# Kernel optimization log

Hardware: AMD Instinct MI355X
Metric: run time of the kernel (lower is better)

The kernel has to match this reference:

```python
import jax, jax.numpy as jnp
import numpy as np

DEPTH = 5
EPS = 1e-8


def setup_inputs() -> dict:
    key = jax.random.key(0)
    ks = jax.random.split(key, 7)
    N, E, Q = 50000, 1600000, 16
    return {
        "marg_i": jax.random.normal(ks[0], (N, Q), dtype=jnp.float32),
        "cav_ij": jax.random.uniform(ks[1], (E, Q), dtype=jnp.float32),
        "C": jax.random.uniform(ks[2], (Q, Q), dtype=jnp.float32),
        "field_i": jax.random.normal(ks[3], (N, Q), dtype=jnp.float32),
        "edge_dst": jax.random.randint(ks[4], (E,), 0, N, dtype=jnp.int32),
        "a1_src": jax.random.randint(ks[5], (E,), 0, N, dtype=jnp.int32),
        "indice_ij": jax.random.randint(ks[6], (E,), 0, E, dtype=jnp.int32),
    }


def reference(marg_i, cav_ij, C, field_i, edge_dst, a1_src, indice_ij):
    # Belief-propagation layers repeated DEPTH times.
    # B_ @ temp2  -> segment_sum of edge messages into destination nodes [N,Q]
    # A1 @ marg_i -> gather of source-node marginal per edge [E,Q]
    N = field_i.shape[0]

    def step(carry, _):
        marg, cav = carry
        temp2 = jnp.log(cav @ C + EPS)                                  # [E,Q]
        marg = jax.ops.segment_sum(temp2, edge_dst, num_segments=N) + field_i  # [N,Q]
        cav = jax.nn.softmax(marg[a1_src] - temp2[indice_ij], axis=1)  # [E,Q]
        return (marg, cav), None

    (marg, cav), _ = jax.lax.scan(step, (marg_i, cav_ij), None, length=DEPTH)
    return jax.nn.log_softmax(marg, axis=1)
```

## Files before the change

### kernel.cpp

```cpp
#include <hip/hip_runtime.h>
#include <hip/hip_fp16.h>

#define Q 16
#define EPS 1e-8f
#define DEPTH 5

typedef unsigned int u32;
typedef _Float16 h2 __attribute__((ext_vector_type(2)));

__device__ __forceinline__ u32 pack2(float a, float b) {
    __half2 h = __floats2half2_rn(a, b);
    return *(u32*)&h;
}
__device__ __forceinline__ float2 unpack2(u32 u) {
    __half2 h = *(__half2*)&u;
    return __half22float2(h);
}
__device__ __forceinline__ h2 mkh2(float a, float b) {
    h2 v; v[0] = (_Float16)a; v[1] = (_Float16)b; return v;
}


__global__ __launch_bounds__(256) void hist_kernel(
    const int* __restrict__ dst, int* __restrict__ count, int E)
{
    int e = blockIdx.x * 256 + threadIdx.x;
    if (e < E) atomicAdd(&count[dst[e]], 1);
}

__global__ __launch_bounds__(256) void scan_partial(
    const int* __restrict__ count, int* __restrict__ partial, int N)
{
    __shared__ int sm[256];
    int i = blockIdx.x * 256 + threadIdx.x;
    sm[threadIdx.x] = (i < N) ? count[i] : 0;
    __syncthreads();
    for (int off = 128; off > 0; off >>= 1) {
        if (threadIdx.x < off) sm[threadIdx.x] += sm[threadIdx.x + off];
        __syncthreads();
    }
    if (threadIdx.x == 0) partial[blockIdx.x] = sm[0];
}

__global__ __launch_bounds__(1024) void scan_top(
    int* __restrict__ partial, int nb)
{
    __shared__ int sm[1024];
    int t = threadIdx.x;
    int v = (t < nb) ? partial[t] : 0;
    sm[t] = v;
    __syncthreads();
    for (int off = 1; off < 1024; off <<= 1) {
        int u = (t >= off) ? sm[t - off] : 0;
        __syncthreads();
        sm[t] += u;
        __syncthreads();
    }
    if (t < nb) partial[t] = sm[t] - v;
}

__global__ __launch_bounds__(256) void scan_final(
    const int* __restrict__ count, const int* __restrict__ partial,
    int* __restrict__ start, int N)
{
    __shared__ int sm[256];
    int i = blockIdx.x * 256 + threadIdx.x;
    int v = (i < N) ? count[i] : 0;
    sm[threadIdx.x] = v;
    __syncthreads();
    for (int off = 1; off < 256; off <<= 1) {
        int u = (threadIdx.x >= off) ? sm[threadIdx.x - off] : 0;
        __syncthreads();
        sm[threadIdx.x] += u;
        __syncthreads();
    }
    int excl = sm[threadIdx.x] - v + partial[blockIdx.x];
    if (i < N) start[i] = excl;
    if (i == N - 1) start[N] = excl + v;
}

__global__ __launch_bounds__(256) void rank_kernel(
    const int* __restrict__ dst, int* __restrict__ cursor,
    int* __restrict__ pos, int E)
{
    int e = blockIdx.x * 256 + threadIdx.x;
    if (e < E) pos[e] = atomicAdd(&cursor[dst[e]], 1);
}

__global__ __launch_bounds__(256) void compose_zip(
    const int* __restrict__ a1_src, const int* __restrict__ indice,
    const int* __restrict__ dst, const int* __restrict__ pos,
    int4* __restrict__ zip, int E)
{
    int e = blockIdx.x * 256 + threadIdx.x;
    if (e < E) zip[e] = make_int4(a1_src[e], pos[indice[e]], dst[e], e);
}

__global__ __launch_bounds__(256) void scatter4(
    const int4* __restrict__ zip, const int* __restrict__ pos,
    int4* __restrict__ sorted, int E)
{
    int e = blockIdx.x * 256 + threadIdx.x;
    if (e < E) sorted[pos[e]] = zip[e];
}

__global__ __launch_bounds__(256) void meta_pack(
    const int4* __restrict__ sorted, int2* __restrict__ meta2, int E)
{
    int j = blockIdx.x * 256 + threadIdx.x;
    if (j < E) {
        int4 m = sorted[j];
        meta2[j] = make_int2(m.y, (m.z << 16) | m.x);
    }
}

__global__ __launch_bounds__(256) void bnode_build(
    const int* __restrict__ start, int* __restrict__ blist,
    int* __restrict__ bcount, int N)
{
    int n = blockIdx.x * 256 + threadIdx.x;
    if (n >= N) return;
    int slo = start[n], shi = start[n + 1];
    bool need = (slo == shi) || ((slo >> 8) != ((shi - 1) >> 8));
    if (need) {
        int p = atomicAdd(bcount, 1);
        blist[p] = n;
    }
}

__global__ __launch_bounds__(256) void binit(
    const int* __restrict__ blist, const int* __restrict__ bcount,
    const float* __restrict__ field, float* __restrict__ marg)
{
    int idx = blockIdx.x * 256 + threadIdx.x;
    int cnt = *bcount;
    if (idx >= cnt * 4) return;
    int n = blist[idx >> 2], part = idx & 3;
    ((float4*)(marg + (size_t)n * Q))[part] =
        ((const float4*)(field + (size_t)n * Q))[part];
}

template<int MODE>
__global__ __launch_bounds__(256) void fused_round(
    const int4* __restrict__ sorted, const int2* __restrict__ meta2,
    const float* __restrict__ C,
    const float* __restrict__ cav,
    const float* __restrict__ marg_in, const u32* __restrict__ t2_old,
    const int* __restrict__ start, const float* __restrict__ field,
    u32* __restrict__ t2_new, float* __restrict__ marg_out, int E)
{
    __shared__ __align__(16) h2 Csh[Q * 8];
    __shared__ float stage[256 * 17];
    __shared__ int s_nfirst, s_nlast;

    const int tid = threadIdx.x;
    const int blo = blockIdx.x * 256;
    const int bhi = min(blo + 256, E);
    if (tid < 128) {
        int q = tid >> 3, kk = tid & 7;
        Csh[q * 8 + kk] = mkh2(C[(2 * kk) * Q + q], C[(2 * kk + 1) * Q + q]);
    }
    if (tid == 0) {
        if (MODE == 0) {
            s_nfirst = sorted[blo].z;
            s_nlast  = sorted[bhi - 1].z;
        } else {
            s_nfirst = ((u32)meta2[blo].y) >> 16;
            s_nlast  = ((u32)meta2[bhi - 1].y) >> 16;
        }
    }
    __syncthreads();

    const int j = blo + tid;
    float t[Q];
    if (j < E) {
        h2 uh[8];
        float s, logs;
        if (MODE == 0) {
            const int e = sorted[j].w;
            const float4* rp = (const float4*)(cav + (size_t)e * Q);
            float4 a0 = rp[0], a1 = rp[1], a2 = rp[2], a3 = rp[3];
            uh[0] = mkh2(a0.x, a0.y); uh[1] = mkh2(a0.z, a0.w);
            uh[2] = mkh2(a1.x, a1.y); uh[3] = mkh2(a1.z, a1.w);
            uh[4] = mkh2(a2.x, a2.y); uh[5] = mkh2(a2.z, a2.w);
            uh[6] = mkh2(a3.x, a3.y); uh[7] = mkh2(a3.z, a3.w);
            s = 1.f; logs = 0.f;
        } else {
            const int2 meta = meta2[j];
            const int src = meta.y & 0xffff;
            const float4* mp = (const float4*)(marg_in + (size_t)src * Q);
            const uint4*  tp = (const uint4*)(t2_old + (size_t)meta.x * 8);
            float4 m0 = mp[0], m1 = mp[1], m2 = mp[2], m3 = mp[3];
            uint4 r0 = tp[0], r1 = tp[1];
            float2 p0 = unpack2(r0.x), p1 = unpack2(r0.y),
                   p2 = unpack2(r0.z), p3 = unpack2(r0.w);
            float2 p4 = unpack2(r1.x), p5 = unpack2(r1.y),
                   p6 = unpack2(r1.z), p7 = unpack2(r1.w);

            float x[Q] = {m0.x - p0.x, m0.y - p0.y, m0.z - p1.x, m0.w - p1.y,
                          m1.x - p2.x, m1.y - p2.y, m1.z - p3.x, m1.w - p3.y,
                          m2.x - p4.x, m2.y - p4.y, m2.z - p5.x, m2.w - p5.y,
                          m3.x - p6.x, m3.y - p6.y, m3.z - p7.x, m3.w - p7.y};

            float mx = x[0];
#pragma unroll
            for (int q = 1; q < Q; ++q) mx = fmaxf(mx, x[q]);
            float u[Q];
            s = 0.f;
#pragma unroll
            for (int q = 0; q < Q; ++q) { u[q] = __expf(x[q] - mx); s += u[q]; }
            logs = __logf(s);
#pragma unroll
            for (int k = 0; k < 8; ++k) uh[k] = mkh2(u[2 * k], u[2 * k + 1]);
        }

        const float base = EPS * s;
#pragma unroll
        for (int q = 0; q < Q; ++q) {
            const uint4* cp = (const uint4*)&Csh[q * 8];
            h2 col[8];
            ((uint4*)col)[0] = cp[0];
            ((uint4*)col)[1] = cp[1];
            float acc = base;
#pragma unroll
            for (int kk = 0; kk < 8; ++kk)
                acc = __builtin_amdgcn_fdot2(uh[kk], col[kk], acc, false);
            t[q] = __logf(acc) - logs;
        }

        if (MODE != 2) {
            uint4 w0, w1;
            w0.x = pack2(t[0],  t[1]);  w0.y = pack2(t[2],  t[3]);
            w0.z = pack2(t[4],  t[5]);  w0.w = pack2(t[6],  t[7]);
            w1.x = pack2(t[8],  t[9]);  w1.y = pack2(t[10], t[11]);
            w1.z = pack2(t[12], t[13]); w1.w = pack2(t[14], t[15]);
            uint4* op = (uint4*)(t2_new + (size_t)j * 8);
            op[0] = w0; op[1] = w1;
        }
    } else {
#pragma unroll
        for (int q = 0; q < Q; ++q) t[q] = 0.f;
    }

#pragma unroll
    for (int q = 0; q < Q; ++q) stage[tid * 17 + q] = t[q];
    __syncthreads();

    const int nfirst = s_nfirst;
    const int ncnt = s_nlast - nfirst + 1;
    for (int k = tid; k < ncnt * Q; k += 256) {
        int ln = k >> 4, q = k & 15;
        int n = nfirst + ln;
        int slo = start[n], shi = start[n + 1];
        int lo = max(slo, blo), hi = min(shi, bhi);
        float s = 0.f;
        for (int sl = lo; sl < hi; ++sl) s += stage[(sl - blo) * 17 + q];
        if (slo >= blo && shi <= bhi)
            marg_out[(size_t)n * Q + q] = s + field[(size_t)n * Q + q];
        else
            atomicAdd(marg_out + (size_t)n * Q + q, s);
    }
}

__global__ __launch_bounds__(256) void node_out(
    const float* __restrict__ marg, float* __restrict__ out, int N)
{
    int i = blockIdx.x * 256 + threadIdx.x;
    if (i >= N) return;

    const float4* mp = (const float4*)(marg + (size_t)i * Q);
    float4 m0 = mp[0], m1 = mp[1], m2 = mp[2], m3 = mp[3];
    float x[Q] = {m0.x, m0.y, m0.z, m0.w, m1.x, m1.y, m1.z, m1.w,
                  m2.x, m2.y, m2.z, m2.w, m3.x, m3.y, m3.z, m3.w};

    float mx = x[0];
#pragma unroll
    for (int q = 1; q < Q; ++q) mx = fmaxf(mx, x[q]);
    float s = 0.f;
#pragma unroll
    for (int q = 0; q < Q; ++q) s += __expf(x[q] - mx);
    float lse = mx + __logf(s);

    float4* op = (float4*)(out + (size_t)i * Q);
    op[0] = make_float4(x[0]  - lse, x[1]  - lse, x[2]  - lse, x[3]  - lse);
    op[1] = make_float4(x[4]  - lse, x[5]  - lse, x[6]  - lse, x[7]  - lse);
    op[2] = make_float4(x[8]  - lse, x[9]  - lse, x[10] - lse, x[11] - lse);
    op[3] = make_float4(x[12] - lse, x[13] - lse, x[14] - lse, x[15] - lse);
}

extern "C" void kernel_launch(void* const* d_in, const int* in_sizes, int n_in,
                              void* d_out, int out_size, void* d_ws, size_t ws_size,
                              hipStream_t stream) {
    const float* cav_in   = (const float*)d_in[1];
    const float* C        = (const float*)d_in[2];
    const float* field_i  = (const float*)d_in[3];
    const int*   edge_dst = (const int*)d_in[4];
    const int*   a1_src   = (const int*)d_in[5];
    const int*   indice   = (const int*)d_in[6];
    float* out = (float*)d_out;

    const int E = in_sizes[4];
    const int N = in_sizes[0] / Q;

    char* ws = (char*)d_ws;
    const size_t t2_bytes   = (size_t)E * 32;
    const size_t i4_bytes   = (size_t)E * 16;
    const size_t node_bytes = (size_t)N * Q * sizeof(float);
    u32*   t2a    = (u32*)ws;                     ws += t2_bytes;
    u32*   t2b    = (u32*)ws;                     ws += t2_bytes;
    int4*  zip    = (int4*)ws;                    ws += i4_bytes;
    int4*  sorted = (int4*)ws;                    ws += i4_bytes;
    int2*  meta2  = (int2*)ws;                    ws += (size_t)E * 8;
    float* marg_a = (float*)ws;                   ws += node_bytes;
    float* marg_b = (float*)ws;                   ws += node_bytes;
    int*   pos    = (int*)ws;                     ws += (size_t)E * 4;
    int*   count  = (int*)ws;                     ws += (size_t)N * 4;
    int*   bcount = (int*)ws;                     ws += 4;
    int*   start  = (int*)ws;                     ws += (size_t)(N + 1) * 4;
    int*   cursor = (int*)ws;                     ws += (size_t)N * 4;
    int*   blist  = (int*)ws;                     ws += (size_t)N * 4;
    int*   partial= (int*)ws;

    const int eb = 256;
    const int eg = (E + eb - 1) / eb;
    const int ng = (N + eb - 1) / eb;

    hipMemsetAsync(count, 0, (size_t)N * 4 + 4, stream);
    hist_kernel<<<eg, eb, 0, stream>>>(edge_dst, count, E);
    scan_partial<<<ng, eb, 0, stream>>>(count, partial, N);
    scan_top<<<1, 1024, 0, stream>>>(partial, ng);
    scan_final<<<ng, eb, 0, stream>>>(count, partial, start, N);
    hipMemcpyAsync(cursor, start, (size_t)N * 4, hipMemcpyDeviceToDevice, stream);
    rank_kernel<<<eg, eb, 0, stream>>>(edge_dst, cursor, pos, E);
    compose_zip<<<eg, eb, 0, stream>>>(a1_src, indice, edge_dst, pos, zip, E);
    scatter4<<<eg, eb, 0, stream>>>(zip, pos, sorted, E);
    meta_pack<<<eg, eb, 0, stream>>>(sorted, meta2, E);
    bnode_build<<<ng, eb, 0, stream>>>(start, blist, bcount, N);

    u32* t_cur = t2a;
    u32* t_nxt = t2b;
    float* m_in = marg_b;
    float* m_out = marg_a;
    const int bg = (N * 4 + eb - 1) / eb;

    for (int it = 0; it < DEPTH; ++it) {
        binit<<<bg, eb, 0, stream>>>(blist, bcount, field_i, m_out);
        if (it == 0)
            fused_round<0><<<eg, eb, 0, stream>>>(sorted, meta2, C, cav_in,
                                                  nullptr, nullptr, start, field_i,
                                                  t_cur, m_out, E);
        else if (it != DEPTH - 1)
            fused_round<1><<<eg, eb, 0, stream>>>(sorted, meta2, C, nullptr,
                                                  m_in, t_cur, start, field_i,
                                                  t_nxt, m_out, E);
        else
            fused_round<2><<<eg, eb, 0, stream>>>(sorted, meta2, C, nullptr,
                                                  m_in, t_cur, start, field_i,
                                                  nullptr, m_out, E);
        if (it != 0) { u32* tt = t_cur; t_cur = t_nxt; t_nxt = tt; }
        float* tm = m_in; m_in = m_out; m_out = tm;
    }

    node_out<<<ng, eb, 0, stream>>>(m_in, out, N);
}
```

Measured before the change: 666.5 us.

## Reuse histogram atomics for ranks, fuse zip+scatter, hoist gathers before sync

The histogram kernel now records each edge's local rank from its atomicAdd. That removes the second atomic rank pass and the cursor memcpy, since the sorted position is now start[dst]+local_rank. The compose_zip and scatter4 kernels are merged into one direct scatter, which drops the zip buffer and one full read and write of E int4. In fused_round, the per-edge global gathers are issued before the shared-memory C load and __syncthreads so their latency overlaps the barrier, and the block's first and last dst come from the threads' own loads.

```diff
diff --git a/kernel.cpp b/kernel.cpp
--- a/kernel.cpp
+++ b/kernel.cpp
@@ -21,11 +21,12 @@
 }
 
 
-__global__ __launch_bounds__(256) void hist_kernel(
-    const int* __restrict__ dst, int* __restrict__ count, int E)
+__global__ __launch_bounds__(256) void rank0_kernel(
+    const int* __restrict__ dst, int* __restrict__ count,
+    int* __restrict__ lr, int E)
 {
     int e = blockIdx.x * 256 + threadIdx.x;
-    if (e < E) atomicAdd(&count[dst[e]], 1);
+    if (e < E) lr[e] = atomicAdd(&count[dst[e]], 1);
 }
 
 __global__ __launch_bounds__(256) void scan_partial(
@@ -79,29 +80,22 @@
     if (i == N - 1) start[N] = excl + v;
 }
 
-__global__ __launch_bounds__(256) void rank_kernel(
-    const int* __restrict__ dst, int* __restrict__ cursor,
-    int* __restrict__ pos, int E)
+__global__ __launch_bounds__(256) void pos_kernel(
+    const int* __restrict__ dst, const int* __restrict__ lr,
+    const int* __restrict__ start, int* __restrict__ pos, int E)
 {
     int e = blockIdx.x * 256 + threadIdx.x;
-    if (e < E) pos[e] = atomicAdd(&cursor[dst[e]], 1);
-}
-
-__global__ __launch_bounds__(256) void compose_zip(
+    if (e < E) pos[e] = start[dst[e]] + lr[e];
+}
+
+__global__ __launch_bounds__(256) void scatter_direct(
     const int* __restrict__ a1_src, const int* __restrict__ indice,
     const int* __restrict__ dst, const int* __restrict__ pos,
-    int4* __restrict__ zip, int E)
+    int4* __restrict__ sorted, int E)
 {
     int e = blockIdx.x * 256 + threadIdx.x;
-    if (e < E) zip[e] = make_int4(a1_src[e], pos[indice[e]], dst[e], e);
-}
-
-__global__ __launch_bounds__(256) void scatter4(
-    const int4* __restrict__ zip, const int* __restrict__ pos,
-    int4* __restrict__ sorted, int E)
-{
-    int e = blockIdx.x * 256 + threadIdx.x;
-    if (e < E) sorted[pos[e]] = zip[e];
+    if (e < E)
+        sorted[pos[e]] = make_int4(a1_src[e], pos[indice[e]], dst[e], e);
 }
 
 __global__ __launch_bounds__(256) void meta_pack(
@@ -156,42 +150,52 @@
     const int tid = threadIdx.x;
     const int blo = blockIdx.x * 256;
     const int bhi = min(blo + 256, E);
+    const int j = blo + tid;
+    const bool act = (j < E);
+
+    int4 smeta;
+    int2 meta;
+    float4 m0, m1, m2, m3;
+    uint4 r0, r1;
+    if (MODE == 0) {
+        if (act) {
+            smeta = sorted[j];
+            const float4* rp = (const float4*)(cav + (size_t)smeta.w * Q);
+            m0 = rp[0]; m1 = rp[1]; m2 = rp[2]; m3 = rp[3];
+        }
+    } else {
+        if (act) {
+            meta = meta2[j];
+            const int src = meta.y & 0xffff;
+            const float4* mp = (const float4*)(marg_in + (size_t)src * Q);
+            const uint4*  tp = (const uint4*)(t2_old + (size_t)meta.x * 8);
+            m0 = mp[0]; m1 = mp[1]; m2 = mp[2]; m3 = mp[3];
+            r0 = tp[0]; r1 = tp[1];
+        }
+    }
+
     if (tid < 128) {
         int q = tid >> 3, kk = tid & 7;
         Csh[q * 8 + kk] = mkh2(C[(2 * kk) * Q + q], C[(2 * kk + 1) * Q + q]);
     }
-    if (tid == 0) {
-        if (MODE == 0) {
-            s_nfirst = sorted[blo].z;
-            s_nlast  = sorted[bhi - 1].z;
-        } else {
-            s_nfirst = ((u32)meta2[blo].y) >> 16;
-            s_nlast  = ((u32)meta2[bhi - 1].y) >> 16;
-        }
-    }
-    __syncthreads();
-
-    const int j = blo + tid;
+    if (act) {
+        int mydst = (MODE == 0) ? smeta.z : (int)(((u32)meta.y) >> 16);
+        if (j == blo)     s_nfirst = mydst;
+        if (j == bhi - 1) s_nlast  = mydst;
+    }
+    __syncthreads();
+
     float t[Q];
-    if (j < E) {
+    if (act) {
         h2 uh[8];
         float s, logs;
         if (MODE == 0) {
-            const int e = sorted[j].w;
-            const float4* rp = (const float4*)(cav + (size_t)e * Q);
-            float4 a0 = rp[0], a1 = rp[1], a2 = rp[2], a3 = rp[3];
-            uh[0] = mkh2(a0.x, a0.y); uh[1] = mkh2(a0.z, a0.w);
-            uh[2] = mkh2(a1.x, a1.y); uh[3] = mkh2(a1.z, a1.w);
-            uh[4] = mkh2(a2.x, a2.y); uh[5] = mkh2(a2.z, a2.w);
-            uh[6] = mkh2(a3.x, a3.y); uh[7] = mkh2(a3.z, a3.w);
+            uh[0] = mkh2(m0.x, m0.y); uh[1] = mkh2(m0.z, m0.w);
+            uh[2] = mkh2(m1.x, m1.y); uh[3] = mkh2(m1.z, m1.w);
+            uh[4] = mkh2(m2.x, m2.y); uh[5] = mkh2(m2.z, m2.w);
+            uh[6] = mkh2(m3.x, m3.y); uh[7] = mkh2(m3.z, m3.w);
             s = 1.f; logs = 0.f;
         } else {
-            const int2 meta = meta2[j];
-            const int src = meta.y & 0xffff;
-            const float4* mp = (const float4*)(marg_in + (size_t)src * Q);
-            const uint4*  tp = (const uint4*)(t2_old + (size_t)meta.x * 8);
-            float4 m0 = mp[0], m1 = mp[1], m2 = mp[2], m3 = mp[3];
-            uint4 r0 = tp[0], r1 = tp[1];
             float2 p0 = unpack2(r0.x), p1 = unpack2(r0.y),
                    p2 = unpack2(r0.z), p3 = unpack2(r0.w);
             float2 p4 = unpack2(r1.x), p5 = unpack2(r1.y),
@@ -308,16 +312,15 @@
     const size_t node_bytes = (size_t)N * Q * sizeof(float);
     u32*   t2a    = (u32*)ws;                     ws += t2_bytes;
     u32*   t2b    = (u32*)ws;                     ws += t2_bytes;
-    int4*  zip    = (int4*)ws;                    ws += i4_bytes;
     int4*  sorted = (int4*)ws;                    ws += i4_bytes;
     int2*  meta2  = (int2*)ws;                    ws += (size_t)E * 8;
     float* marg_a = (float*)ws;                   ws += node_bytes;
     float* marg_b = (float*)ws;                   ws += node_bytes;
     int*   pos    = (int*)ws;                     ws += (size_t)E * 4;
+    int*   lr     = (int*)ws;                     ws += (size_t)E * 4;
     int*   count  = (int*)ws;                     ws += (size_t)N * 4;
     int*   bcount = (int*)ws;                     ws += 4;
     int*   start  = (int*)ws;                     ws += (size_t)(N + 1) * 4;
-    int*   cursor = (int*)ws;                     ws += (size_t)N * 4;
     int*   blist  = (int*)ws;                     ws += (size_t)N * 4;
     int*   partial= (int*)ws;
 
@@ -326,14 +329,12 @@
     const int ng = (N + eb - 1) / eb;
 
     hipMemsetAsync(count, 0, (size_t)N * 4 + 4, stream);
-    hist_kernel<<<eg, eb, 0, stream>>>(edge_dst, count, E);
+    rank0_kernel<<<eg, eb, 0, stream>>>(edge_dst, count, lr, E);
     scan_partial<<<ng, eb, 0, stream>>>(count, partial, N);
     scan_top<<<1, 1024, 0, stream>>>(partial, ng);
     scan_final<<<ng, eb, 0, stream>>>(count, partial, start, N);
-    hipMemcpyAsync(cursor, start, (size_t)N * 4, hipMemcpyDeviceToDevice, stream);
-    rank_kernel<<<eg, eb, 0, stream>>>(edge_dst, cursor, pos, E);
-    compose_zip<<<eg, eb, 0, stream>>>(a1_src, indice, edge_dst, pos, zip, E);
-    scatter4<<<eg, eb, 0, stream>>>(zip, pos, sorted, E);
+    pos_kernel<<<eg, eb, 0, stream>>>(edge_dst, lr, start, pos, E);
+    scatter_direct<<<eg, eb, 0, stream>>>(a1_src, indice, edge_dst, pos, sorted, E);
     meta_pack<<<eg, eb, 0, stream>>>(sorted, meta2, E);
     bnode_build<<<ng, eb, 0, stream>>>(start, blist, bcount, N);
 
```

After: 608.1 us. -8.8%, faster.
